# Kernel tuning notes

Measured on AMD Instinct MI355X. Metric: run time of the kernel, lower is better.

The kernel has to match this reference:

```python
import jax, jax.numpy as jnp
import numpy as np

N_NODES = 50000
N_EDGES = 800000
N_SUPPORTS = 2
D_IN = 512
D_OUT = 128


def setup_inputs() -> dict:
    key = jax.random.key(0)
    ks = jax.random.split(key, 6)
    x = jax.random.normal(ks[0], (N_NODES, D_IN), dtype=jnp.float32)
    kernels = jax.random.normal(ks[1], (N_SUPPORTS, D_IN, D_OUT), dtype=jnp.float32) * 0.05
    bias = jax.random.normal(ks[2], (D_OUT,), dtype=jnp.float32) * 0.05
    adj_vals = jax.random.uniform(ks[3], (N_SUPPORTS, N_EDGES), dtype=jnp.float32)
    adj_rows = jax.random.randint(ks[4], (N_SUPPORTS, N_EDGES), 0, N_NODES, dtype=jnp.int32)
    adj_cols = jax.random.randint(ks[5], (N_SUPPORTS, N_EDGES), 0, N_NODES, dtype=jnp.int32)
    return {"x": x, "kernels": kernels, "bias": bias,
            "adj_vals": adj_vals, "adj_rows": adj_rows, "adj_cols": adj_cols}


def _spmm(vals, rows, cols, dense):
    # COO sparse [N,N] @ dense [N,F] -> [N,F]
    gathered = vals[:, None] * dense[cols]            # [E, F]
    return jax.ops.segment_sum(gathered, rows, num_segments=N_NODES)


def reference(x, kernels, bias, adj_vals, adj_rows, adj_cols):
    # dropout rate = 0.0 -> identity
    out = jnp.zeros((N_NODES, D_OUT), dtype=x.dtype)
    for s in range(N_SUPPORTS):  # small fixed number of supports
        pre_sup = x @ kernels[s]                      # [N, D_OUT]
        out = out + _spmm(adj_vals[s], adj_rows[s], adj_cols[s], pre_sup)
    out = out + bias
    return jax.nn.relu(out)
```

## Files before the change

### kernel.cpp

```cpp
#include <hip/hip_runtime.h>

#define N_NODES 50000
#define N_EDGES 800000
#define D_IN    512
#define D_OUT   128
#define N_SUP   2
#define N_COLS  (N_SUP * D_OUT)
#define NB_S    782
#define NB      (N_SUP * NB_S)
#define CAPF    1280
#define CHUNK   3125
#define TILE_R  16
#define NTILES  (N_NODES / TILE_R)
#define GGRID   256

typedef __attribute__((ext_vector_type(8))) __bf16 bf16x8;
typedef __attribute__((ext_vector_type(4))) float  f32x4;

__global__ __launch_bounds__(256) void convert_w(const float* __restrict__ w,
                                                 __bf16* __restrict__ wt2,
                                                 int* __restrict__ gcursor) {
    const int g = blockIdx.x * 256 + threadIdx.x;
    if (g < NB) gcursor[g] = 0;
    if (g >= (D_IN / 8) * N_COLS) return;
    const int kq = g >> 8;
    const int n  = g & 255;
    const int s  = n >> 7;
    const int np = n & 127;
    bf16x8 v;
#pragma unroll
    for (int j = 0; j < 8; ++j)
        v[j] = (__bf16)w[((size_t)s * D_IN + kq * 8 + j) * D_OUT + np];
    *(bf16x8*)(wt2 + (size_t)g * 8) = v;
}

__global__ __launch_bounds__(512, 2) void gemm_bf16_v2(const float* __restrict__ x,
                                                       const __bf16* __restrict__ wt2,
                                                       __bf16* __restrict__ pre) {
    __shared__ __align__(16) __bf16 As[TILE_R * 64 * 8];

    const int t    = threadIdx.x;
    const int lane = t & 63;
    const int w    = t >> 6;
    const int l15  = lane & 15;
    const int quad = lane >> 4;

    bf16x8 B0[16], B1[16];
#pragma unroll
    for (int kb = 0; kb < 16; ++kb) {
        const size_t g0 = (size_t)(kb * 4 + quad) * 256 + w * 32 + l15;
        B0[kb] = *(const bf16x8*)(wt2 + g0 * 8);
        B1[kb] = *(const bf16x8*)(wt2 + (g0 + 16) * 8);
    }

    const int s_out = w >> 2;
    const int cp0   = (w & 3) * 32 + l15;

    const int srow = t >> 5;
    const int sc0  = (t & 31) * 2;
    const int swz  = srow & 7;

    int tile = blockIdx.x;
    float4 f0, f1, f2, f3;
    {
        const float* src = x + ((size_t)tile * TILE_R + srow) * D_IN + sc0 * 8;
        f0 = ((const float4*)src)[0];
        f1 = ((const float4*)src)[1];
        f2 = ((const float4*)src)[2];
        f3 = ((const float4*)src)[3];
    }

    while (tile < NTILES) {
        bf16x8 lo, hi;
        lo[0] = (__bf16)f0.x; lo[1] = (__bf16)f0.y; lo[2] = (__bf16)f0.z; lo[3] = (__bf16)f0.w;
        lo[4] = (__bf16)f1.x; lo[5] = (__bf16)f1.y; lo[6] = (__bf16)f1.z; lo[7] = (__bf16)f1.w;
        hi[0] = (__bf16)f2.x; hi[1] = (__bf16)f2.y; hi[2] = (__bf16)f2.z; hi[3] = (__bf16)f2.w;
        hi[4] = (__bf16)f3.x; hi[5] = (__bf16)f3.y; hi[6] = (__bf16)f3.z; hi[7] = (__bf16)f3.w;

        __syncthreads();
        *(bf16x8*)&As[((size_t)srow * 64 + (sc0       ^ swz)) * 8] = lo;
        *(bf16x8*)&As[((size_t)srow * 64 + ((sc0 + 1) ^ swz)) * 8] = hi;
        __syncthreads();

        const int next = tile + GGRID;
        if (next < NTILES) {
            const float* src = x + ((size_t)next * TILE_R + srow) * D_IN + sc0 * 8;
            f0 = ((const float4*)src)[0];
            f1 = ((const float4*)src)[1];
            f2 = ((const float4*)src)[2];
            f3 = ((const float4*)src)[3];
        }

        f32x4 acc0 = (f32x4)0.f, acc1 = (f32x4)0.f;
#pragma unroll
        for (int kb = 0; kb < 16; ++kb) {
            const int c = (kb * 4 + quad) ^ (l15 & 7);
            bf16x8 a = *(const bf16x8*)&As[((size_t)l15 * 64 + c) * 8];
            acc0 = __builtin_amdgcn_mfma_f32_16x16x32_bf16(a, B0[kb], acc0, 0, 0, 0);
            acc1 = __builtin_amdgcn_mfma_f32_16x16x32_bf16(a, B1[kb], acc1, 0, 0, 0);
        }

        __bf16* dst = pre + ((size_t)s_out * N_NODES + (size_t)tile * TILE_R + quad * 4) * D_OUT + cp0;
#pragma unroll
        for (int r = 0; r < 4; ++r) {
            dst[(size_t)r * D_OUT]      = (__bf16)acc0[r];
            dst[(size_t)r * D_OUT + 16] = (__bf16)acc1[r];
        }

        tile = next;
    }
}

__global__ __launch_bounds__(512) void scatter_coarse(const float* __restrict__ adj_vals,
                                                      const int* __restrict__ adj_rows,
                                                      const int* __restrict__ adj_cols,
                                                      int* __restrict__ gcursor,
                                                      uint2* __restrict__ coarse) {
    __shared__ int hist[NB_S];
    __shared__ int excl[NB_S];
    __shared__ int lbase[NB_S];
    __shared__ int rankc[NB_S];
    __shared__ int sc[1024];
    __shared__ uint2 buf[CHUNK];

    const int bid = blockIdx.x;
    const int s   = bid >> 8;
    const int ch  = bid & 255;
    const int t   = threadIdx.x;

    for (int b = t; b < NB_S; b += 512) { hist[b] = 0; rankc[b] = 0; }
    __syncthreads();

    const int e0 = ch * CHUNK;
    int   rr[7]; int cc[7]; float vv[7];
#pragma unroll
    for (int i = 0; i < 7; ++i) {
        const int idx = i * 512 + t;
        if (idx < CHUNK) {
            const size_t src = (size_t)s * N_EDGES + e0 + idx;
            rr[i] = adj_rows[src];
            cc[i] = adj_cols[src];
            vv[i] = adj_vals[src];
            atomicAdd(&hist[rr[i] >> 6], 1);
        } else {
            rr[i] = -1; cc[i] = 0; vv[i] = 0.f;
        }
    }
    __syncthreads();

    sc[t]       = (t       < NB_S) ? hist[t]       : 0;
    sc[t + 512] = (t + 512 < NB_S) ? hist[t + 512] : 0;
    __syncthreads();
    for (int off = 1; off < 1024; off <<= 1) {
        const int a0 = (t >= off) ? sc[t - off] : 0;
        const int a1 = sc[t + 512 - off];
        __syncthreads();
        sc[t]       += a0;
        sc[t + 512] += a1;
        __syncthreads();
    }
#pragma unroll
    for (int h = 0; h < 2; ++h) {
        const int b = t + h * 512;
        if (b < NB_S) {
            excl[b]  = sc[b] - hist[b];
            lbase[b] = hist[b] ? atomicAdd(&gcursor[s * NB_S + b], hist[b]) : 0;
        }
    }
    __syncthreads();

#pragma unroll
    for (int i = 0; i < 7; ++i) {
        if (rr[i] >= 0) {
            const int b   = rr[i] >> 6;
            const int pos = excl[b] + atomicAdd(&rankc[b], 1);
            buf[pos] = make_uint2(__float_as_uint(vv[i]),
                                  ((unsigned)rr[i] << 16) | (unsigned)cc[i]);
        }
    }
    __syncthreads();

    for (int i = t; i < CHUNK; i += 512) {
        const uint2 ed = buf[i];
        const int b   = (int)(ed.y >> 22);
        const int dst = lbase[b] + (i - excl[b]);
        if (dst < CAPF)
            coarse[(size_t)(s * NB_S + b) * CAPF + dst] = ed;
    }
}

__global__ __launch_bounds__(512) void fine_gather(const uint2* __restrict__ coarse,
                                                   const int* __restrict__ gcursor,
                                                   const uint4* __restrict__ pre_q,
                                                   const float* __restrict__ bias,
                                                   float* __restrict__ out) {
    __shared__ uint2 buf[2 * CAPF];
    __shared__ int rex[2][64];
    __shared__ int rcnt[2][64];
    __shared__ int rh[64];
    __shared__ int rc[64];
    __shared__ int sd[64];

    const int bk = blockIdx.x;
    const int t  = threadIdx.x;

#pragma unroll
    for (int s = 0; s < N_SUP; ++s) {
        if (t < 64) { rh[t] = 0; rc[t] = 0; }
        __syncthreads();

        const int bkt  = s * NB_S + bk;
        const size_t b0 = (size_t)bkt * CAPF;
        const int cnt  = min(gcursor[bkt], CAPF);

        uint2 ev0, ev1, ev2;
        ev0 = make_uint2(0u, 0u); ev1 = ev0; ev2 = ev0;
        if (t < cnt)        { ev0 = coarse[b0 + t];        atomicAdd(&rh[(ev0.y >> 16) & 63], 1); }
        if (t + 512 < cnt)  { ev1 = coarse[b0 + t + 512];  atomicAdd(&rh[(ev1.y >> 16) & 63], 1); }
        if (t + 1024 < cnt) { ev2 = coarse[b0 + t + 1024]; atomicAdd(&rh[(ev2.y >> 16) & 63], 1); }
        __syncthreads();

        if (t < 64) sd[t] = rh[t];
        __syncthreads();
        for (int off = 1; off < 64; off <<= 1) {
            const int a = (t < 64 && t >= off) ? sd[t - off] : 0;
            __syncthreads();
            if (t < 64) sd[t] += a;
            __syncthreads();
        }
        if (t < 64) {
            rex[s][t]  = sd[t] - rh[t];
            rcnt[s][t] = rh[t];
        }
        __syncthreads();

        if (t < cnt) {
            const int rl = (ev0.y >> 16) & 63;
            buf[s * CAPF + rex[s][rl] + atomicAdd(&rc[rl], 1)] =
                make_uint2(ev0.x, ev0.y & 0xFFFFu);
        }
        if (t + 512 < cnt) {
            const int rl = (ev1.y >> 16) & 63;
            buf[s * CAPF + rex[s][rl] + atomicAdd(&rc[rl], 1)] =
                make_uint2(ev1.x, ev1.y & 0xFFFFu);
        }
        if (t + 1024 < cnt) {
            const int rl = (ev2.y >> 16) & 63;
            buf[s * CAPF + rex[s][rl] + atomicAdd(&rc[rl], 1)] =
                make_uint2(ev2.x, ev2.y & 0xFFFFu);
        }
        __syncthreads();
    }

    const int lane = t & 63;
    const int q    = lane >> 4;
    const int fl   = lane & 15;
    const int wv   = t >> 6;

    for (int ri = 0; ri < 8; ++ri) {
        const int rloc = wv * 8 + ri;
        const int row  = bk * 64 + rloc;

        float a[8];
#pragma unroll
        for (int k = 0; k < 8; ++k) a[k] = 0.f;

#pragma unroll
        for (int s = 0; s < N_SUP; ++s) {
            const int start = rex[s][rloc];
            const int cnt   = rcnt[s][rloc];
            const uint2* eb = buf + s * CAPF + start;
            const uint4* psup = pre_q + (size_t)s * N_NODES * 16 + fl;

            for (int e0 = 0; e0 < cnt; e0 += 64) {
                const int m = min(64, cnt - e0);
                int   c = 0;
                float v = 0.f;
                if (lane < m) {
                    const uint2 ed = eb[e0 + lane];
                    v = __uint_as_float(ed.x);
                    c = (int)ed.y;
                }
                const int steps = (m + 3) >> 2;

                auto step = [&](int jj) {
                    const int   idx = (jj < m) ? jj : 0;
                    float vj = __shfl(v, idx);
                    const int cj = __shfl(c, idx);
                    if (jj >= m) vj = 0.f;
                    const uint4 p = psup[(size_t)cj * 16];
                    a[0] += vj * __uint_as_float(p.x << 16);
                    a[1] += vj * __uint_as_float(p.x & 0xffff0000u);
                    a[2] += vj * __uint_as_float(p.y << 16);
                    a[3] += vj * __uint_as_float(p.y & 0xffff0000u);
                    a[4] += vj * __uint_as_float(p.z << 16);
                    a[5] += vj * __uint_as_float(p.z & 0xffff0000u);
                    a[6] += vj * __uint_as_float(p.w << 16);
                    a[7] += vj * __uint_as_float(p.w & 0xffff0000u);
                };
                int jj = 0;
                for (; jj + 1 < steps; jj += 2) {
                    step(jj * 4 + q);
                    step(jj * 4 + 4 + q);
                }
                if (jj < steps) step(jj * 4 + q);
            }
        }

#pragma unroll
        for (int k = 0; k < 8; ++k) {
            a[k] += __shfl_xor(a[k], 16);
            a[k] += __shfl_xor(a[k], 32);
        }

        if (lane < 16 && row < N_NODES) {
            const float4 b0 = *(const float4*)(bias + fl * 8);
            const float4 b1 = *(const float4*)(bias + fl * 8 + 4);
            float4 o0, o1;
            o0.x = fmaxf(a[0] + b0.x, 0.f);
            o0.y = fmaxf(a[1] + b0.y, 0.f);
            o0.z = fmaxf(a[2] + b0.z, 0.f);
            o0.w = fmaxf(a[3] + b0.w, 0.f);
            o1.x = fmaxf(a[4] + b1.x, 0.f);
            o1.y = fmaxf(a[5] + b1.y, 0.f);
            o1.z = fmaxf(a[6] + b1.z, 0.f);
            o1.w = fmaxf(a[7] + b1.w, 0.f);
            float* dst = out + (size_t)row * D_OUT + fl * 8;
            *(float4*)(dst)     = o0;
            *(float4*)(dst + 4) = o1;
        }
    }
}

extern "C" void kernel_launch(void* const* d_in, const int* in_sizes, int n_in,
                              void* d_out, int out_size, void* d_ws, size_t ws_size,
                              hipStream_t stream) {
    const float* x        = (const float*)d_in[0];
    const float* kernels  = (const float*)d_in[1];
    const float* bias     = (const float*)d_in[2];
    const float* adj_vals = (const float*)d_in[3];
    const int*   adj_rows = (const int*)d_in[4];
    const int*   adj_cols = (const int*)d_in[5];
    float* out = (float*)d_out;

    char* ws = (char*)d_ws;
    size_t off = 0;
    auto alloc = [&](size_t bytes) {
        char* p = ws + off;
        off += (bytes + 255) & ~(size_t)255;
        return p;
    };
    __bf16* pre    = (__bf16*)alloc(sizeof(__bf16) * N_SUP * N_NODES * D_OUT);
    __bf16* wt2    = (__bf16*)alloc(sizeof(__bf16) * D_IN * N_COLS);
    uint2*  coarse = (uint2*) alloc(sizeof(uint2)  * NB * CAPF);
    int*    gcursor = (int*)alloc(sizeof(int) * NB);

    convert_w<<<(D_IN / 8) * N_COLS / 256, 256, 0, stream>>>(kernels, wt2, gcursor);

    gemm_bf16_v2<<<GGRID, 512, 0, stream>>>(x, wt2, pre);

    scatter_coarse<<<512, 512, 0, stream>>>(adj_vals, adj_rows, adj_cols,
                                            gcursor, coarse);

    fine_gather<<<NB_S, 512, 0, stream>>>(coarse, gcursor, (const uint4*)pre,
                                          bias, out);
}
```

Before: 261.3 us.

## Fuse weight conversion into GEMM and double-buffer LDS with two-tile prefetch

Drops the separate convert_w launch: each GEMM thread now loads its fp32 weight fragments directly and converts them to bf16 in registers, and block 0 zeroes the cursor array. The A tile in LDS is double-buffered, so one barrier per iteration replaces two, and x rows are prefetched two tiles ahead instead of one. This saves a kernel launch and some synchronisation, at the cost of strided fp32 weight reads repeated across all 256 blocks and more registers for the extra prefetch set.

New measurement: 283.9 us. 1.09x slower.

```diff
diff --git a/kernel.cpp b/kernel.cpp
--- a/kernel.cpp
+++ b/kernel.cpp
@@ -17,85 +17,86 @@
 typedef __attribute__((ext_vector_type(8))) __bf16 bf16x8;
 typedef __attribute__((ext_vector_type(4))) float  f32x4;
 
-__global__ __launch_bounds__(256) void convert_w(const float* __restrict__ w,
-                                                 __bf16* __restrict__ wt2,
-                                                 int* __restrict__ gcursor) {
-    const int g = blockIdx.x * 256 + threadIdx.x;
-    if (g < NB) gcursor[g] = 0;
-    if (g >= (D_IN / 8) * N_COLS) return;
-    const int kq = g >> 8;
-    const int n  = g & 255;
-    const int s  = n >> 7;
-    const int np = n & 127;
-    bf16x8 v;
-#pragma unroll
-    for (int j = 0; j < 8; ++j)
-        v[j] = (__bf16)w[((size_t)s * D_IN + kq * 8 + j) * D_OUT + np];
-    *(bf16x8*)(wt2 + (size_t)g * 8) = v;
-}
-
-__global__ __launch_bounds__(512, 2) void gemm_bf16_v2(const float* __restrict__ x,
-                                                       const __bf16* __restrict__ wt2,
-                                                       __bf16* __restrict__ pre) {
-    __shared__ __align__(16) __bf16 As[TILE_R * 64 * 8];
+__global__ __launch_bounds__(512, 2) void gemm_bf16_v3(const float* __restrict__ x,
+                                                       const float* __restrict__ w,
+                                                       __bf16* __restrict__ pre,
+                                                       int* __restrict__ gcursor) {
+    __shared__ __align__(16) __bf16 As[2][TILE_R * 64 * 8];
 
     const int t    = threadIdx.x;
     const int lane = t & 63;
-    const int w    = t >> 6;
+    const int wv   = t >> 6;
     const int l15  = lane & 15;
     const int quad = lane >> 4;
 
+    if (blockIdx.x == 0)
+        for (int i = t; i < NB; i += 512) gcursor[i] = 0;
+
+    const int n  = wv * 32 + l15;
+    const int sb = n >> 7;
+    const int np = n & 127;
     bf16x8 B0[16], B1[16];
 #pragma unroll
     for (int kb = 0; kb < 16; ++kb) {
-        const size_t g0 = (size_t)(kb * 4 + quad) * 256 + w * 32 + l15;
-        B0[kb] = *(const bf16x8*)(wt2 + g0 * 8);
-        B1[kb] = *(const bf16x8*)(wt2 + (g0 + 16) * 8);
-    }
-
-    const int s_out = w >> 2;
-    const int cp0   = (w & 3) * 32 + l15;
+        const float* wp = w + ((size_t)sb * D_IN + (kb * 4 + quad) * 8) * D_OUT + np;
+#pragma unroll
+        for (int j = 0; j < 8; ++j) {
+            B0[kb][j] = (__bf16)wp[(size_t)j * D_OUT];
+            B1[kb][j] = (__bf16)wp[(size_t)j * D_OUT + 16];
+        }
+    }
+
+    const int s_out = wv >> 2;
+    const int cp0   = (wv & 3) * 32 + l15;
 
     const int srow = t >> 5;
     const int sc0  = (t & 31) * 2;
     const int swz  = srow & 7;
 
     int tile = blockIdx.x;
-    float4 f0, f1, f2, f3;
+    float4 a0, a1, a2, a3;
+    float4 b0, b1, b2, b3;
     {
         const float* src = x + ((size_t)tile * TILE_R + srow) * D_IN + sc0 * 8;
-        f0 = ((const float4*)src)[0];
-        f1 = ((const float4*)src)[1];
-        f2 = ((const float4*)src)[2];
-        f3 = ((const float4*)src)[3];
-    }
-
+        a0 = ((const float4*)src)[0];
+        a1 = ((const float4*)src)[1];
+        a2 = ((const float4*)src)[2];
+        a3 = ((const float4*)src)[3];
+    }
+    if (tile + GGRID < NTILES) {
+        const float* src = x + ((size_t)(tile + GGRID) * TILE_R + srow) * D_IN + sc0 * 8;
+        b0 = ((const float4*)src)[0];
+        b1 = ((const float4*)src)[1];
+        b2 = ((const float4*)src)[2];
+        b3 = ((const float4*)src)[3];
+    }
+
+    int nb = 0;
     while (tile < NTILES) {
         bf16x8 lo, hi;
-        lo[0] = (__bf16)f0.x; lo[1] = (__bf16)f0.y; lo[2] = (__bf16)f0.z; lo[3] = (__bf16)f0.w;
-        lo[4] = (__bf16)f1.x; lo[5] = (__bf16)f1.y; lo[6] = (__bf16)f1.z; lo[7] = (__bf16)f1.w;
-        hi[0] = (__bf16)f2.x; hi[1] = (__bf16)f2.y; hi[2] = (__bf16)f2.z; hi[3] = (__bf16)f2.w;
-        hi[4] = (__bf16)f3.x; hi[5] = (__bf16)f3.y; hi[6] = (__bf16)f3.z; hi[7] = (__bf16)f3.w;
-
-        __syncthreads();
-        *(bf16x8*)&As[((size_t)srow * 64 + (sc0       ^ swz)) * 8] = lo;
-        *(bf16x8*)&As[((size_t)srow * 64 + ((sc0 + 1) ^ swz)) * 8] = hi;
-        __syncthreads();
-
-        const int next = tile + GGRID;
-        if (next < NTILES) {
-            const float* src = x + ((size_t)next * TILE_R + srow) * D_IN + sc0 * 8;
-            f0 = ((const float4*)src)[0];
-            f1 = ((const float4*)src)[1];
-            f2 = ((const float4*)src)[2];
-            f3 = ((const float4*)src)[3];
-        }
+        lo[0] = (__bf16)a0.x; lo[1] = (__bf16)a0.y; lo[2] = (__bf16)a0.z; lo[3] = (__bf16)a0.w;
+        lo[4] = (__bf16)a1.x; lo[5] = (__bf16)a1.y; lo[6] = (__bf16)a1.z; lo[7] = (__bf16)a1.w;
+        hi[0] = (__bf16)a2.x; hi[1] = (__bf16)a2.y; hi[2] = (__bf16)a2.z; hi[3] = (__bf16)a2.w;
+        hi[4] = (__bf16)a3.x; hi[5] = (__bf16)a3.y; hi[6] = (__bf16)a3.z; hi[7] = (__bf16)a3.w;
+        *(bf16x8*)&As[nb][((size_t)srow * 64 + (sc0       ^ swz)) * 8] = lo;
+        *(bf16x8*)&As[nb][((size_t)srow * 64 + ((sc0 + 1) ^ swz)) * 8] = hi;
+
+        a0 = b0; a1 = b1; a2 = b2; a3 = b3;
+        if (tile + 2 * GGRID < NTILES) {
+            const float* src = x + ((size_t)(tile + 2 * GGRID) * TILE_R + srow) * D_IN + sc0 * 8;
+            b0 = ((const float4*)src)[0];
+            b1 = ((const float4*)src)[1];
+            b2 = ((const float4*)src)[2];
+            b3 = ((const float4*)src)[3];
+        }
+
+        __syncthreads();
 
         f32x4 acc0 = (f32x4)0.f, acc1 = (f32x4)0.f;
 #pragma unroll
         for (int kb = 0; kb < 16; ++kb) {
             const int c = (kb * 4 + quad) ^ (l15 & 7);
-            bf16x8 a = *(const bf16x8*)&As[((size_t)l15 * 64 + c) * 8];
+            bf16x8 a = *(const bf16x8*)&As[nb][((size_t)l15 * 64 + c) * 8];
             acc0 = __builtin_amdgcn_mfma_f32_16x16x32_bf16(a, B0[kb], acc0, 0, 0, 0);
             acc1 = __builtin_amdgcn_mfma_f32_16x16x32_bf16(a, B1[kb], acc1, 0, 0, 0);
         }
@@ -107,7 +108,8 @@
             dst[(size_t)r * D_OUT + 16] = (__bf16)acc1[r];
         }
 
-        tile = next;
+        tile += GGRID;
+        nb ^= 1;
     }
 }
 
@@ -351,13 +353,10 @@
         return p;
     };
     __bf16* pre    = (__bf16*)alloc(sizeof(__bf16) * N_SUP * N_NODES * D_OUT);
-    __bf16* wt2    = (__bf16*)alloc(sizeof(__bf16) * D_IN * N_COLS);
     uint2*  coarse = (uint2*) alloc(sizeof(uint2)  * NB * CAPF);
     int*    gcursor = (int*)alloc(sizeof(int) * NB);
 
-    convert_w<<<(D_IN / 8) * N_COLS / 256, 256, 0, stream>>>(kernels, wt2, gcursor);
-
-    gemm_bf16_v2<<<GGRID, 512, 0, stream>>>(x, wt2, pre);
+    gemm_bf16_v3<<<GGRID, 512, 0, stream>>>(x, kernels, pre, gcursor);
 
     scatter_coarse<<<512, 512, 0, stream>>>(adj_vals, adj_rows, adj_cols,
                                             gcursor, coarse);
```
